# Kernel tuning notes

Hardware: AMD Instinct MI355X
Metric: run time of the kernel (lower is better)

The kernel has to match this reference:

```python
import jax, jax.numpy as jnp
import numpy as np

B, N, C, L, O = 32, 16000, 128, 512, 35
FS = 16000
F_LO, F_HI = 100.0, 8000.0
BETA = 0.9        # Leaky decay (snntorch Leaky beta)
AN_UTH = 0.5      # auditory-nerve threshold (an_uth)
TH = 1.0          # default threshold for later stages
STELI_STD = (1.0, 2.0, 3.0)


def _gammatone_kernels():
    # 4th-order gammatone impulse responses, ERB-spaced center freqs.
    erb = lambda f: 21.4 * np.log10(4.37 * f / 1000.0 + 1.0)
    erb_inv = lambda e: (10 ** (e / 21.4) - 1.0) * 1000.0 / 4.37
    cfs = erb_inv(np.linspace(erb(F_LO), erb(F_HI), C))          # [C]
    t = np.arange(L) / FS                                        # [L]
    bw = 1.019 * 24.7 * (4.37 * cfs / 1000.0 + 1.0)              # [C]
    g = (t[None, :] ** 3) * np.exp(-2 * np.pi * bw[:, None] * t[None, :]) \
        * np.cos(2 * np.pi * cfs[:, None] * t[None, :])          # [C,L]
    g = g / np.maximum(np.linalg.norm(g, axis=1, keepdims=True), 1e-12)
    return jnp.asarray(g, dtype=jnp.float32)


def _gauss_w(std, n):
    # fixed Gaussian lateral connectivity (OSF / stellate layer)
    i = np.arange(n, dtype=np.float64)
    w = np.exp(-((i[:, None] - i[None, :]) ** 2) / (2.0 * std ** 2))
    w = w / w.sum(axis=1, keepdims=True)
    return jnp.asarray(w, dtype=jnp.float32)


@jax.custom_vjp
def spike(x):
    return (x > 0).astype(x.dtype)

def _spk_fwd(x):
    return spike(x), x

def _spk_bwd(x, g):
    # ATan-style surrogate gradient (snntorch default)
    return (g / (1.0 + (jnp.pi * x) ** 2),)

spike.defvjp(_spk_fwd, _spk_bwd)


def setup_inputs() -> dict:
    key = jax.random.key(0)
    ks = jax.random.split(key, 8)
    s = 1.0 / np.sqrt(C)
    return {
        "audio": jax.random.normal(ks[0], (B, N), jnp.float32),
        "gt_kernels": _gammatone_kernels(),
        "W_an": jax.random.normal(ks[1], (C, C), jnp.float32) * s,
        "b_an": jnp.zeros((C,), jnp.float32),
        "W_b": _gauss_w(STELI_STD[0], C),
        "W_m": _gauss_w(STELI_STD[1], C),
        "W_n": _gauss_w(STELI_STD[2], C),
        "W_ic": jax.random.normal(ks[2], (C, C), jnp.float32) * s,
        "b_ic": jnp.zeros((C,), jnp.float32),
        "W_ac": jax.random.normal(ks[3], (O, C), jnp.float32) * s,
        "b_ac": jnp.zeros((O,), jnp.float32),
        "ihc_win": 160,
    }


def reference(audio, gt_kernels, W_an, b_an, W_b, W_m, W_n, W_ic, b_ic, W_ac, b_ac, ihc_win):
    # Cochlea: gammatone FIR filterbank.  [B,N] -> [B,C,N]
    x = jax.lax.conv_general_dilated(
        audio[:, None, :], gt_kernels[:, None, :], (1,), "SAME",
        dimension_numbers=("NCH", "OIH", "NCH"))
    # Inner hair cell: half-wave rectify + windowed average (envelope, downsample)
    x = jax.nn.relu(x)
    T = N // ihc_win
    x = x[..., : T * ihc_win].reshape(B, C, T, ihc_win).mean(-1)   # [B,C,T]
    x = x.transpose(2, 0, 1)                                       # [T,B,C]

    def leaky(mem, cur, th):
        mem = BETA * mem + cur
        spk = spike(mem - th)
        return spk, mem - spk * th   # reset by subtraction

    def step(carry, xt):
        m_an, m_b, m_m, m_n, m_ic, m_ac = carry
        s_an, m_an = leaky(m_an, xt @ W_an.T + b_an, AN_UTH)
        s_b,  m_b  = leaky(m_b,  s_an @ W_b.T, TH)
        s_m,  m_m  = leaky(m_m,  s_b @ W_m.T, TH)
        s_n,  m_n  = leaky(m_n,  s_m @ W_n.T, TH)
        s_ic, m_ic = leaky(m_ic, s_n @ W_ic.T + b_ic, TH)
        s_ac, m_ac = leaky(m_ac, s_ic @ W_ac.T + b_ac, TH)
        return (m_an, m_b, m_m, m_n, m_ic, m_ac), (s_ac, m_ac)

    z = jnp.zeros((B, C), x.dtype)
    za = jnp.zeros((B, O), x.dtype)
    _, (spk_rec, mem_rec) = jax.lax.scan(step, (z, z, z, z, z, za), x)
    # [T,B,O] -> [B,T,O]; stack (spk, mem) like the torch module's tuple output
    return jnp.stack([spk_rec.transpose(1, 0, 2), mem_rec.transpose(1, 0, 2)])
```

## Files before the change

### kernel.cpp

```cpp
#include <hip/hip_runtime.h>
#include <math.h>

#define BB 32
#define NN 16000
#define CC 128
#define LL 512
#define OO 35
#define TT 100
#define BTO (BB * TT * OO)
#define FSR 16000.0

#define SEG 640
#define NSEG 25
#define SPAN 1153

#define WT_OFF   0
#define PAR_OFF  0x100000
#define CUR_OFF  0
#define XT_OFF   0x350000

__global__ __launch_bounds__(512) void gt_tables(double* __restrict__ Wt,
                                                 double* __restrict__ par) {
    const int c = blockIdx.x;
    const int l = threadIdx.x;
    const double TWO_PI = 6.283185307179586476925287;
    const double e_lo = 21.4 * log10(4.37 * 100.0 / 1000.0 + 1.0);
    const double e_hi = 21.4 * log10(4.37 * 8000.0 / 1000.0 + 1.0);
    const double step = (e_hi - e_lo) / 127.0;
    const double e = (c == 127) ? e_hi : e_lo + c * step;
    const double cf = (pow(10.0, e / 21.4) - 1.0) * 1000.0 / 4.37;
    const double bw = 1.019 * 24.7 * (4.37 * cf / 1000.0 + 1.0);

    const double t = (double)l / FSR;
    const double env = exp(-TWO_PI * bw * t);
    const double ang = TWO_PI * cf * t;
    const double wr = env * cos(ang);
    const double wi = env * sin(ang);
    Wt[(l * CC + c) * 2 + 0] = wr;
    Wt[(l * CC + c) * 2 + 1] = wi;

    __shared__ double red[512];
    const double l3 = (double)l * (double)l * (double)l;
    const double q = l3 * wr;
    red[l] = q * q;
    __syncthreads();
    for (int s = 256; s > 0; s >>= 1) {
        if (l < s) red[l] += red[l + s];
        __syncthreads();
    }
    if (l == 0) {
        double* p = par + c * 16;
        const double a1 = TWO_PI * bw / FSR, th1 = TWO_PI * cf / FSR;
        const double e1 = exp(-a1);
        p[0] = e1 * cos(th1);
        p[1] = e1 * sin(th1);
        const double aL = TWO_PI * bw * (512.0 / FSR), thL = TWO_PI * cf * (512.0 / FSR);
        const double eL = exp(-aL);
        const double pr = eL * cos(thL), pim = eL * sin(thL);
        p[2] = pr;              p[3] = pim;
        p[4] = 512.0 * pr;      p[5] = 512.0 * pim;
        p[6] = 130816.0 * pr;   p[7] = 130816.0 * pim;
        p[8] = 22238720.0 * pr; p[9] = 22238720.0 * pim;
        p[10] = 1.0 / sqrt(red[0]);
    }
}

__global__ __launch_bounds__(128) void conv_rec(
    const float* __restrict__ audio,
    const double* __restrict__ Wt,
    const double* __restrict__ par,
    float* __restrict__ xt)
{
    const int blk = blockIdx.x;
    const int b = blk / NSEG;
    const int seg = blk % NSEG;
    const int n0 = seg * SEG;
    const int c = threadIdx.x;

    __shared__ float alds[SPAN];
    for (int i = c; i < SPAN; i += 128) {
        const int g = n0 - 256 + i;
        alds[i] = (g >= 0 && g < NN) ? audio[b * NN + g] : 0.0f;
    }
    __syncthreads();

    const double* p = par + c * 16;
    const double rr = p[0], ri = p[1];
    const double cr0 = p[2], ci0 = p[3], cr1 = p[4], ci1 = p[5];
    const double cr2 = p[6], ci2 = p[7], cr3 = p[8], ci3 = p[9];
    const double scale = p[10];

    double d0r = 0, d0i = 0, d1r = 0, d1i = 0, d2r = 0, d2i = 0, d3r = 0, d3i = 0;
    #pragma unroll 4
    for (int l = 0; l < 512; ++l) {
        const double wr = Wt[(l * CC + c) * 2 + 0];
        const double wi = Wt[(l * CC + c) * 2 + 1];
        const double av = (double)alds[SEG + 1 + l];
        const double bl = (double)l;
        const double b2 = bl * (bl - 1.0) * 0.5;
        const double b3 = b2 * (bl - 2.0) * (1.0 / 3.0);
        d0r = fma(wr, av, d0r);              d0i = fma(wi, av, d0i);
        const double t1 = av * bl;
        d1r = fma(wr, t1, d1r);              d1i = fma(wi, t1, d1i);
        const double t2 = av * b2;
        d2r = fma(wr, t2, d2r);              d2i = fma(wi, t2, d2i);
        const double t3 = av * b3;
        d3r = fma(wr, t3, d3r);              d3i = fma(wi, t3, d3i);
    }

    double wsum = 0.0;
    int widx = (b * TT + seg * 4 + 3) * CC + c;
    int cnt = 0;
    #pragma unroll 2
    for (int m = 0; m < SEG; ++m) {
        const int li = SEG - m;
        const double ain  = (double)alds[li];
        const double aout = (double)alds[li + 512];
        const double t3r = d3r + d2r, t3i = d3i + d2i;
        const double t2r = d2r + d1r, t2i = d2i + d1i;
        const double t1r = d1r + d0r, t1i = d1i + d0i;
        d3r = fma(t3r, rr, fma(t3i, -ri, -cr3 * aout));
        d3i = fma(t3r, ri, fma(t3i,  rr, -ci3 * aout));
        d2r = fma(t2r, rr, fma(t2i, -ri, -cr2 * aout));
        d2i = fma(t2r, ri, fma(t2i,  rr, -ci2 * aout));
        d1r = fma(t1r, rr, fma(t1i, -ri, -cr1 * aout));
        d1i = fma(t1r, ri, fma(t1i,  rr, -ci1 * aout));
        const double o0r = fma(d0r, rr, fma(d0i, -ri, fma(-cr0, aout, ain)));
        const double o0i = fma(d0r, ri, fma(d0i,  rr, -ci0 * aout));
        d0r = o0r; d0i = o0i;
        const double yv = scale * fma(6.0, d2r + d3r, d1r);
        float yf = (float)yv;
        yf = yf > 0.0f ? yf : 0.0f;
        wsum += (double)yf;
        if (++cnt == 160) {
            xt[widx] = (float)(wsum / 160.0);
            widx -= CC;
            wsum = 0.0;
            cnt = 0;
        }
    }
}

__global__ __launch_bounds__(128) void an_cur_kernel(
    const float* __restrict__ xt, const float* __restrict__ W_an,
    const float* __restrict__ b_an, double* __restrict__ cur_d)
{
    __shared__ float xr[CC];
    const int row = blockIdx.x;
    const int c = threadIdx.x;
    xr[c] = xt[row * CC + c];
    __syncthreads();
    const float* wr = W_an + c * CC;
    double acc = (double)b_an[c];
    #pragma unroll
    for (int k = 0; k < CC; k += 4) {
        float4 w4 = *reinterpret_cast<const float4*>(wr + k);
        acc += (double)w4.x * (double)xr[k]
             + (double)w4.y * (double)xr[k+1]
             + (double)w4.z * (double)xr[k+2]
             + (double)w4.w * (double)xr[k+3];
    }
    cur_d[row * CC + c] = acc;
}

#define R1 8
#define W1 17
#define R2 16
#define W2 33
#define R3 24
#define W3 49
#define SPW 24

__global__ __launch_bounds__(512, 1) void snn_kernel(
    const double* __restrict__ cur_an,
    const float* __restrict__ W_b, const float* __restrict__ W_m, const float* __restrict__ W_n,
    const float* __restrict__ W_ic, const float* __restrict__ b_ic,
    const float* __restrict__ W_ac, const float* __restrict__ b_ac,
    float* __restrict__ out)
{
    __shared__ __align__(16) float sa[2][176], sb[2][176], sm[2][176];
    __shared__ __align__(16) float sn_[2][CC];
    __shared__ __align__(16) double icp[2][4][CC];
    __shared__ __align__(16) float sic[2][CC];
    __shared__ double acp[2][2][36];
    __shared__ __align__(16) float wac[OO][132];

    const int b = blockIdx.x;
    const int tid = threadIdx.x;
    const int wid = tid >> 6;
    const int l = tid & 63;
    const int c0 = 2 * l, c1 = 2 * l + 1;

    {
        float* z0 = &sa[0][0]; float* z1 = &sb[0][0]; float* z2 = &sm[0][0];
        for (int i = tid; i < 352; i += 512) { z0[i] = 0.f; z1[i] = 0.f; z2[i] = 0.f; }
    }
    for (int i = tid; i < OO * CC; i += 512)
        wac[i >> 7][i & 127] = W_ac[i];

    float wband[2 * W3];
    double bic0 = 0.0, bic1 = 0.0, bacv = 0.0;
    double mm0 = 0.0, mm1 = 0.0;
    double mic0 = 0.0, mic1 = 0.0;
    double macv = 0.0;
    double2 pf0 = make_double2(0.0, 0.0), pf1 = make_double2(0.0, 0.0);

    if (wid == 0) {
        pf0 = *reinterpret_cast<const double2*>(&cur_an[(b * TT + 0) * CC + c0]);
        pf1 = *reinterpret_cast<const double2*>(&cur_an[(b * TT + 1) * CC + c0]);
        bic0 = (double)b_ic[c0]; bic1 = (double)b_ic[c1];
        if (l < OO) bacv = (double)b_ac[l];
    } else if (wid == 1) {
        #pragma unroll
        for (int x = 0; x < W1; ++x) {
            int k0 = c0 - R1 + x, k1 = c1 - R1 + x;
            wband[x]      = (k0 >= 0 && k0 < CC) ? W_b[c0 * CC + k0] : 0.f;
            wband[W1 + x] = (k1 >= 0 && k1 < CC) ? W_b[c1 * CC + k1] : 0.f;
        }
    } else if (wid == 2) {
        #pragma unroll
        for (int x = 0; x < W2; ++x) {
            int k0 = c0 - R2 + x, k1 = c1 - R2 + x;
            wband[x]      = (k0 >= 0 && k0 < CC) ? W_m[c0 * CC + k0] : 0.f;
            wband[W2 + x] = (k1 >= 0 && k1 < CC) ? W_m[c1 * CC + k1] : 0.f;
        }
    } else if (wid == 3) {
        #pragma unroll
        for (int x = 0; x < W3; ++x) {
            int k0 = c0 - R3 + x, k1 = c1 - R3 + x;
            wband[x]      = (k0 >= 0 && k0 < CC) ? W_n[c0 * CC + k0] : 0.f;
            wband[W3 + x] = (k1 >= 0 && k1 < CC) ? W_n[c1 * CC + k1] : 0.f;
        }
    } else {
        const int q = wid - 4;
        #pragma unroll
        for (int j = 0; j < 32; ++j) {
            wband[j]      = W_ic[c0 * CC + 32 * q + j];
            wband[32 + j] = W_ic[c1 * CC + 32 * q + j];
        }
    }
    __syncthreads();

    for (int tick = 0; tick < TT + 7; ++tick) {
        if (wid == 0) {
            if (tick < TT) {
                double2 cv = pf0; pf0 = pf1;
                if (tick + 2 < TT)
                    pf1 = *reinterpret_cast<const double2*>(&cur_an[(b * TT + tick + 2) * CC + c0]);
                double me0 = 0.9 * mm0 + cv.x; double d0 = me0 - 0.5;
                bool s0 = d0 > 0.0; mm0 = s0 ? d0 : me0;
                double me1 = 0.9 * mm1 + cv.y; double d1 = me1 - 0.5;
                bool s1 = d1 > 0.0; mm1 = s1 ? d1 : me1;
                *reinterpret_cast<float2*>(&sa[tick & 1][SPW + c0]) =
                    make_float2(s0 ? 1.f : 0.f, s1 ? 1.f : 0.f);
            }
            const int t5 = tick - 5;
            if (t5 >= 0 && t5 < TT) {
                const int p = t5 & 1;
                double2 q0 = *reinterpret_cast<const double2*>(&icp[p][0][c0]);
                double2 q1 = *reinterpret_cast<const double2*>(&icp[p][1][c0]);
                double2 q2 = *reinterpret_cast<const double2*>(&icp[p][2][c0]);
                double2 q3 = *reinterpret_cast<const double2*>(&icp[p][3][c0]);
                double acc0 = ((q0.x + q1.x) + (q2.x + q3.x)) + bic0;
                double acc1 = ((q0.y + q1.y) + (q2.y + q3.y)) + bic1;
                double mem0 = 0.9 * mic0 + acc0; double dd0 = mem0 - 1.0;
                bool s0 = dd0 > 0.0; mic0 = s0 ? dd0 : mem0;
                double mem1 = 0.9 * mic1 + acc1; double dd1 = mem1 - 1.0;
                bool s1 = dd1 > 0.0; mic1 = s1 ? dd1 : mem1;
                *reinterpret_cast<float2*>(&sic[p][c0]) =
                    make_float2(s0 ? 1.f : 0.f, s1 ? 1.f : 0.f);
            }
            const int t7 = tick - 7;
            if (l < OO && t7 >= 0 && t7 < TT) {
                const int p = t7 & 1;
                double acc = (acp[p][0][l] + acp[p][1][l]) + bacv;
                double mem = 0.9 * macv + acc;
                double d = mem - 1.0; bool s = d > 0.0;
                macv = s ? d : mem;
                const int idx = (b * TT + t7) * OO + l;
                out[idx] = s ? 1.f : 0.f;
                out[BTO + idx] = (float)macv;
            }
        } else if (wid == 1) {
            const int t = tick - 1;
            if (t >= 0 && t < TT) {
                const int p = t & 1;
                const float2* pw = reinterpret_cast<const float2*>(&sa[p][SPW + c0 - R1]);
                double aA0 = 0, aA1 = 0, aB0 = 0, aB1 = 0;
                #pragma unroll
                for (int i = 0; i < 9; ++i) {
                    float2 v = pw[i];
                    double vx = (double)v.x, vy = (double)v.y;
                    if (2 * i < W1)     aA0 = fma((double)wband[2 * i],          vx, aA0);
                    if (2 * i + 1 < W1) aA1 = fma((double)wband[2 * i + 1],      vy, aA1);
                    if (2 * i >= 1)     aB0 = fma((double)wband[W1 + 2 * i - 1], vx, aB0);
                    if (2 * i < W1)     aB1 = fma((double)wband[W1 + 2 * i],     vy, aB1);
                }
                double me0 = 0.9 * mm0 + (aA0 + aA1); double d0 = me0 - 1.0;
                bool s0 = d0 > 0.0; mm0 = s0 ? d0 : me0;
                double me1 = 0.9 * mm1 + (aB0 + aB1); double d1 = me1 - 1.0;
                bool s1 = d1 > 0.0; mm1 = s1 ? d1 : me1;
                *reinterpret_cast<float2*>(&sb[p][SPW + c0]) =
                    make_float2(s0 ? 1.f : 0.f, s1 ? 1.f : 0.f);
            }
            const int t6 = tick - 6;
            if (t6 >= 0 && t6 < TT) {
                const int p = t6 & 1, r = l >> 1, h = l & 1;
                const float* sp = &sic[p][h * 64];
                const float* wr = &wac[r][h * 64];
                double a0 = 0, a1 = 0, a2 = 0, a3 = 0;
                #pragma unroll
                for (int k = 0; k < 64; k += 4) {
                    float4 v = *reinterpret_cast<const float4*>(&sp[k]);
                    float4 w = *reinterpret_cast<const float4*>(&wr[k]);
                    a0 = fma((double)w.x, (double)v.x, a0);
                    a1 = fma((double)w.y, (double)v.y, a1);
                    a2 = fma((double)w.z, (double)v.z, a2);
                    a3 = fma((double)w.w, (double)v.w, a3);
                }
                acp[p][h][r] = (a0 + a1) + (a2 + a3);
            }
        } else if (wid == 2) {
            const int t = tick - 2;
            if (t >= 0 && t < TT) {
                const int p = t & 1;
                const float2* pw = reinterpret_cast<const float2*>(&sb[p][SPW + c0 - R2]);
                double aA0 = 0, aA1 = 0, aB0 = 0, aB1 = 0;
                #pragma unroll
                for (int i = 0; i < 17; ++i) {
                    float2 v = pw[i];
                    double vx = (double)v.x, vy = (double)v.y;
                    if (2 * i < W2)     aA0 = fma((double)wband[2 * i],          vx, aA0);
                    if (2 * i + 1 < W2) aA1 = fma((double)wband[2 * i + 1],      vy, aA1);
                    if (2 * i >= 1)     aB0 = fma((double)wband[W2 + 2 * i - 1], vx, aB0);
                    if (2 * i < W2)     aB1 = fma((double)wband[W2 + 2 * i],     vy, aB1);
                }
                double me0 = 0.9 * mm0 + (aA0 + aA1); double d0 = me0 - 1.0;
                bool s0 = d0 > 0.0; mm0 = s0 ? d0 : me0;
                double me1 = 0.9 * mm1 + (aB0 + aB1); double d1 = me1 - 1.0;
                bool s1 = d1 > 0.0; mm1 = s1 ? d1 : me1;
                *reinterpret_cast<float2*>(&sm[p][SPW + c0]) =
                    make_float2(s0 ? 1.f : 0.f, s1 ? 1.f : 0.f);
            }
            const int t6 = tick - 6;
            if (l < 6 && t6 >= 0 && t6 < TT) {
                const int p = t6 & 1, r = 32 + (l >> 1), h = l & 1;
                const float* sp = &sic[p][h * 64];
                const float* wr = &wac[r][h * 64];
                double a0 = 0, a1 = 0, a2 = 0, a3 = 0;
                #pragma unroll
                for (int k = 0; k < 64; k += 4) {
                    float4 v = *reinterpret_cast<const float4*>(&sp[k]);
                    float4 w = *reinterpret_cast<const float4*>(&wr[k]);
                    a0 = fma((double)w.x, (double)v.x, a0);
                    a1 = fma((double)w.y, (double)v.y, a1);
                    a2 = fma((double)w.z, (double)v.z, a2);
                    a3 = fma((double)w.w, (double)v.w, a3);
                }
                acp[p][h][r] = (a0 + a1) + (a2 + a3);
            }
        } else if (wid == 3) {
            const int t = tick - 3;
            if (t >= 0 && t < TT) {
                const int p = t & 1;
                const float2* pw = reinterpret_cast<const float2*>(&sm[p][SPW + c0 - R3]);
                double aA0 = 0, aA1 = 0, aB0 = 0, aB1 = 0;
                #pragma unroll
                for (int i = 0; i < 25; ++i) {
                    float2 v = pw[i];
                    double vx = (double)v.x, vy = (double)v.y;
                    if (2 * i < W3)     aA0 = fma((double)wband[2 * i],          vx, aA0);
                    if (2 * i + 1 < W3) aA1 = fma((double)wband[2 * i + 1],      vy, aA1);
                    if (2 * i >= 1)     aB0 = fma((double)wband[W3 + 2 * i - 1], vx, aB0);
                    if (2 * i < W3)     aB1 = fma((double)wband[W3 + 2 * i],     vy, aB1);
                }
                double me0 = 0.9 * mm0 + (aA0 + aA1); double d0 = me0 - 1.0;
                bool s0 = d0 > 0.0; mm0 = s0 ? d0 : me0;
                double me1 = 0.9 * mm1 + (aB0 + aB1); double d1 = me1 - 1.0;
                bool s1 = d1 > 0.0; mm1 = s1 ? d1 : me1;
                *reinterpret_cast<float2*>(&sn_[p][c0]) =
                    make_float2(s0 ? 1.f : 0.f, s1 ? 1.f : 0.f);
            }
        } else {
            const int t = tick - 4;
            if (t >= 0 && t < TT) {
                const int p = t & 1, q = wid - 4;
                const float* sp = &sn_[p][32 * q];
                double a0 = 0, a1 = 0, g0 = 0, g1 = 0;
                #pragma unroll
                for (int k = 0; k < 32; k += 4) {
                    float4 v = *reinterpret_cast<const float4*>(&sp[k]);
                    a0 = fma((double)wband[k],          (double)v.x, a0);
                    a1 = fma((double)wband[k + 1],      (double)v.y, a1);
                    a0 = fma((double)wband[k + 2],      (double)v.z, a0);
                    a1 = fma((double)wband[k + 3],      (double)v.w, a1);
                    g0 = fma((double)wband[32 + k],     (double)v.x, g0);
                    g1 = fma((double)wband[32 + k + 1], (double)v.y, g1);
                    g0 = fma((double)wband[32 + k + 2], (double)v.z, g0);
                    g1 = fma((double)wband[32 + k + 3], (double)v.w, g1);
                }
                *reinterpret_cast<double2*>(&icp[p][q][c0]) =
                    make_double2(a0 + a1, g0 + g1);
            }
        }
        __syncthreads();
    }
}

extern "C" void kernel_launch(void* const* d_in, const int* in_sizes, int n_in,
                              void* d_out, int out_size, void* d_ws, size_t ws_size,
                              hipStream_t stream) {
    const float* audio = (const float*)d_in[0];
    const float* W_an  = (const float*)d_in[2];
    const float* b_an  = (const float*)d_in[3];
    const float* W_b   = (const float*)d_in[4];
    const float* W_m   = (const float*)d_in[5];
    const float* W_n   = (const float*)d_in[6];
    const float* W_ic  = (const float*)d_in[7];
    const float* b_ic  = (const float*)d_in[8];
    const float* W_ac  = (const float*)d_in[9];
    const float* b_ac  = (const float*)d_in[10];

    char* ws = (char*)d_ws;
    double* Wt    = (double*)(ws + WT_OFF);
    double* par   = (double*)(ws + PAR_OFF);
    double* cur_d = (double*)(ws + CUR_OFF);
    float*  xt    = (float*)(ws + XT_OFF);
    float*  out   = (float*)d_out;

    gt_tables<<<dim3(CC), dim3(512), 0, stream>>>(Wt, par);
    conv_rec<<<dim3(BB * NSEG), dim3(128), 0, stream>>>(audio, Wt, par, xt);
    an_cur_kernel<<<dim3(BB * TT), dim3(128), 0, stream>>>(xt, W_an, b_an, cur_d);
    snn_kernel<<<dim3(BB), dim3(512), 0, stream>>>(
        cur_d, W_b, W_m, W_n, W_ic, b_ic, W_ac, b_ac, out);
}
```

Measured before the change: 330.9 us.

## Store SNN spikes and W_ac as double in LDS, strength-reduce binomial weights

In the gammatone init loop the binomial coefficients are now updated incrementally instead of being recomputed per tap, and the complex weight pair is read with one double2 load. The recursion loop unroll goes from 2 to 4. In the SNN kernel the shared spike buffers and W_ac copy are widened to double, which removes float-to-double conversions in the inner products. The leftover W_ac rows are moved from warp 2 to warp 0. The cost is double the LDS footprint and bandwidth for those buffers.

```diff
diff --git a/kernel.cpp b/kernel.cpp
--- a/kernel.cpp
+++ b/kernel.cpp
@@ -91,27 +91,25 @@
     const double scale = p[10];
 
     double d0r = 0, d0i = 0, d1r = 0, d1i = 0, d2r = 0, d2i = 0, d3r = 0, d3i = 0;
+    double b1 = 0.0, b2 = 0.0, b3 = 0.0;
     #pragma unroll 4
     for (int l = 0; l < 512; ++l) {
-        const double wr = Wt[(l * CC + c) * 2 + 0];
-        const double wi = Wt[(l * CC + c) * 2 + 1];
+        const double2 w = *reinterpret_cast<const double2*>(&Wt[(l * CC + c) * 2]);
         const double av = (double)alds[SEG + 1 + l];
-        const double bl = (double)l;
-        const double b2 = bl * (bl - 1.0) * 0.5;
-        const double b3 = b2 * (bl - 2.0) * (1.0 / 3.0);
-        d0r = fma(wr, av, d0r);              d0i = fma(wi, av, d0i);
-        const double t1 = av * bl;
-        d1r = fma(wr, t1, d1r);              d1i = fma(wi, t1, d1i);
+        d0r = fma(w.x, av, d0r);             d0i = fma(w.y, av, d0i);
+        const double t1 = av * b1;
+        d1r = fma(w.x, t1, d1r);             d1i = fma(w.y, t1, d1i);
         const double t2 = av * b2;
-        d2r = fma(wr, t2, d2r);              d2i = fma(wi, t2, d2i);
+        d2r = fma(w.x, t2, d2r);             d2i = fma(w.y, t2, d2i);
         const double t3 = av * b3;
-        d3r = fma(wr, t3, d3r);              d3i = fma(wi, t3, d3i);
+        d3r = fma(w.x, t3, d3r);             d3i = fma(w.y, t3, d3i);
+        b3 += b2; b2 += b1; b1 += 1.0;
     }
 
     double wsum = 0.0;
     int widx = (b * TT + seg * 4 + 3) * CC + c;
     int cnt = 0;
-    #pragma unroll 2
+    #pragma unroll 4
     for (int m = 0; m < SEG; ++m) {
         const int li = SEG - m;
         const double ain  = (double)alds[li];
@@ -178,12 +176,12 @@
     const float* __restrict__ W_ac, const float* __restrict__ b_ac,
     float* __restrict__ out)
 {
-    __shared__ __align__(16) float sa[2][176], sb[2][176], sm[2][176];
-    __shared__ __align__(16) float sn_[2][CC];
+    __shared__ __align__(16) double sa[2][176], sb[2][176], sm[2][176];
+    __shared__ __align__(16) double sn_[2][CC];
     __shared__ __align__(16) double icp[2][4][CC];
-    __shared__ __align__(16) float sic[2][CC];
+    __shared__ __align__(16) double sic[2][CC];
     __shared__ double acp[2][2][36];
-    __shared__ __align__(16) float wac[OO][132];
+    __shared__ __align__(16) double wacd[OO][132];
 
     const int b = blockIdx.x;
     const int tid = threadIdx.x;
@@ -192,11 +190,11 @@
     const int c0 = 2 * l, c1 = 2 * l + 1;
 
     {
-        float* z0 = &sa[0][0]; float* z1 = &sb[0][0]; float* z2 = &sm[0][0];
-        for (int i = tid; i < 352; i += 512) { z0[i] = 0.f; z1[i] = 0.f; z2[i] = 0.f; }
+        double* z0 = &sa[0][0]; double* z1 = &sb[0][0]; double* z2 = &sm[0][0];
+        for (int i = tid; i < 352; i += 512) { z0[i] = 0.0; z1[i] = 0.0; z2[i] = 0.0; }
     }
     for (int i = tid; i < OO * CC; i += 512)
-        wac[i >> 7][i & 127] = W_ac[i];
+        wacd[i >> 7][i & 127] = (double)W_ac[i];
 
     float wband[2 * W3];
     double bic0 = 0.0, bic1 = 0.0, bacv = 0.0;
@@ -251,8 +249,8 @@
                 bool s0 = d0 > 0.0; mm0 = s0 ? d0 : me0;
                 double me1 = 0.9 * mm1 + cv.y; double d1 = me1 - 0.5;
                 bool s1 = d1 > 0.0; mm1 = s1 ? d1 : me1;
-                *reinterpret_cast<float2*>(&sa[tick & 1][SPW + c0]) =
-                    make_float2(s0 ? 1.f : 0.f, s1 ? 1.f : 0.f);
+                *reinterpret_cast<double2*>(&sa[tick & 1][SPW + c0]) =
+                    make_double2(s0 ? 1.0 : 0.0, s1 ? 1.0 : 0.0);
             }
             const int t5 = tick - 5;
             if (t5 >= 0 && t5 < TT) {
@@ -267,8 +265,27 @@
                 bool s0 = dd0 > 0.0; mic0 = s0 ? dd0 : mem0;
                 double mem1 = 0.9 * mic1 + acc1; double dd1 = mem1 - 1.0;
                 bool s1 = dd1 > 0.0; mic1 = s1 ? dd1 : mem1;
-                *reinterpret_cast<float2*>(&sic[p][c0]) =
-                    make_float2(s0 ? 1.f : 0.f, s1 ? 1.f : 0.f);
+                *reinterpret_cast<double2*>(&sic[p][c0]) =
+                    make_double2(s0 ? 1.0 : 0.0, s1 ? 1.0 : 0.0);
+            }
+            const int t6 = tick - 6;
+            if (l < 6 && t6 >= 0 && t6 < TT) {
+                const int p = t6 & 1, r = 32 + (l >> 1), h = l & 1;
+                const double* sp = &sic[p][h * 64];
+                const double* wr = &wacd[r][h * 64];
+                double a0 = 0, a1 = 0, a2 = 0, a3 = 0;
+                #pragma unroll
+                for (int k = 0; k < 64; k += 4) {
+                    double2 v01 = *reinterpret_cast<const double2*>(&sp[k]);
+                    double2 v23 = *reinterpret_cast<const double2*>(&sp[k + 2]);
+                    double2 w01 = *reinterpret_cast<const double2*>(&wr[k]);
+                    double2 w23 = *reinterpret_cast<const double2*>(&wr[k + 2]);
+                    a0 = fma(w01.x, v01.x, a0);
+                    a1 = fma(w01.y, v01.y, a1);
+                    a2 = fma(w23.x, v23.x, a2);
+                    a3 = fma(w23.y, v23.y, a3);
+                }
+                acp[p][h][r] = (a0 + a1) + (a2 + a3);
             }
             const int t7 = tick - 7;
             if (l < OO && t7 >= 0 && t7 < TT) {
@@ -285,12 +302,12 @@
             const int t = tick - 1;
             if (t >= 0 && t < TT) {
                 const int p = t & 1;
-                const float2* pw = reinterpret_cast<const float2*>(&sa[p][SPW + c0 - R1]);
+                const double2* pw = reinterpret_cast<const double2*>(&sa[p][SPW + c0 - R1]);
                 double aA0 = 0, aA1 = 0, aB0 = 0, aB1 = 0;
                 #pragma unroll
                 for (int i = 0; i < 9; ++i) {
-                    float2 v = pw[i];
-                    double vx = (double)v.x, vy = (double)v.y;
+                    double2 v = pw[i];
+                    double vx = v.x, vy = v.y;
                     if (2 * i < W1)     aA0 = fma((double)wband[2 * i],          vx, aA0);
                     if (2 * i + 1 < W1) aA1 = fma((double)wband[2 * i + 1],      vy, aA1);
                     if (2 * i >= 1)     aB0 = fma((double)wband[W1 + 2 * i - 1], vx, aB0);
@@ -300,23 +317,25 @@
                 bool s0 = d0 > 0.0; mm0 = s0 ? d0 : me0;
                 double me1 = 0.9 * mm1 + (aB0 + aB1); double d1 = me1 - 1.0;
                 bool s1 = d1 > 0.0; mm1 = s1 ? d1 : me1;
-                *reinterpret_cast<float2*>(&sb[p][SPW + c0]) =
-                    make_float2(s0 ? 1.f : 0.f, s1 ? 1.f : 0.f);
+                *reinterpret_cast<double2*>(&sb[p][SPW + c0]) =
+                    make_double2(s0 ? 1.0 : 0.0, s1 ? 1.0 : 0.0);
             }
             const int t6 = tick - 6;
             if (t6 >= 0 && t6 < TT) {
                 const int p = t6 & 1, r = l >> 1, h = l & 1;
-                const float* sp = &sic[p][h * 64];
-                const float* wr = &wac[r][h * 64];
+                const double* sp = &sic[p][h * 64];
+                const double* wr = &wacd[r][h * 64];
                 double a0 = 0, a1 = 0, a2 = 0, a3 = 0;
                 #pragma unroll
                 for (int k = 0; k < 64; k += 4) {
-                    float4 v = *reinterpret_cast<const float4*>(&sp[k]);
-                    float4 w = *reinterpret_cast<const float4*>(&wr[k]);
-                    a0 = fma((double)w.x, (double)v.x, a0);
-                    a1 = fma((double)w.y, (double)v.y, a1);
-                    a2 = fma((double)w.z, (double)v.z, a2);
-                    a3 = fma((double)w.w, (double)v.w, a3);
+                    double2 v01 = *reinterpret_cast<const double2*>(&sp[k]);
+                    double2 v23 = *reinterpret_cast<const double2*>(&sp[k + 2]);
+                    double2 w01 = *reinterpret_cast<const double2*>(&wr[k]);
+                    double2 w23 = *reinterpret_cast<const double2*>(&wr[k + 2]);
+                    a0 = fma(w01.x, v01.x, a0);
+                    a1 = fma(w01.y, v01.y, a1);
+                    a2 = fma(w23.x, v23.x, a2);
+                    a3 = fma(w23.y, v23.y, a3);
                 }
                 acp[p][h][r] = (a0 + a1) + (a2 + a3);
             }
@@ -324,12 +343,12 @@
             const int t = tick - 2;
             if (t >= 0 && t < TT) {
                 const int p = t & 1;
-                const float2* pw = reinterpret_cast<const float2*>(&sb[p][SPW + c0 - R2]);
+                const double2* pw = reinterpret_cast<const double2*>(&sb[p][SPW + c0 - R2]);
                 double aA0 = 0, aA1 = 0, aB0 = 0, aB1 = 0;
                 #pragma unroll
                 for (int i = 0; i < 17; ++i) {
-                    float2 v = pw[i];
-                    double vx = (double)v.x, vy = (double)v.y;
+                    double2 v = pw[i];
+                    double vx = v.x, vy = v.y;
                     if (2 * i < W2)     aA0 = fma((double)wband[2 * i],          vx, aA0);
                     if (2 * i + 1 < W2) aA1 = fma((double)wband[2 * i + 1],      vy, aA1);
                     if (2 * i >= 1)     aB0 = fma((double)wband[W2 + 2 * i - 1], vx, aB0);
@@ -339,36 +358,19 @@
                 bool s0 = d0 > 0.0; mm0 = s0 ? d0 : me0;
                 double me1 = 0.9 * mm1 + (aB0 + aB1); double d1 = me1 - 1.0;
                 bool s1 = d1 > 0.0; mm1 = s1 ? d1 : me1;
-                *reinterpret_cast<float2*>(&sm[p][SPW + c0]) =
-                    make_float2(s0 ? 1.f : 0.f, s1 ? 1.f : 0.f);
-            }
-            const int t6 = tick - 6;
-            if (l < 6 && t6 >= 0 && t6 < TT) {
-                const int p = t6 & 1, r = 32 + (l >> 1), h = l & 1;
-                const float* sp = &sic[p][h * 64];
-                const float* wr = &wac[r][h * 64];
-                double a0 = 0, a1 = 0, a2 = 0, a3 = 0;
-                #pragma unroll
-                for (int k = 0; k < 64; k += 4) {
-                    float4 v = *reinterpret_cast<const float4*>(&sp[k]);
-                    float4 w = *reinterpret_cast<const float4*>(&wr[k]);
-                    a0 = fma((double)w.x, (double)v.x, a0);
-                    a1 = fma((double)w.y, (double)v.y, a1);
-                    a2 = fma((double)w.z, (double)v.z, a2);
-                    a3 = fma((double)w.w, (double)v.w, a3);
-                }
-                acp[p][h][r] = (a0 + a1) + (a2 + a3);
+                *reinterpret_cast<double2*>(&sm[p][SPW + c0]) =
+                    make_double2(s0 ? 1.0 : 0.0, s1 ? 1.0 : 0.0);
             }
         } else if (wid == 3) {
             const int t = tick - 3;
             if (t >= 0 && t < TT) {
                 const int p = t & 1;
-                const float2* pw = reinterpret_cast<const float2*>(&sm[p][SPW + c0 - R3]);
+                const double2* pw = reinterpret_cast<const double2*>(&sm[p][SPW + c0 - R3]);
                 double aA0 = 0, aA1 = 0, aB0 = 0, aB1 = 0;
                 #pragma unroll
                 for (int i = 0; i < 25; ++i) {
-                    float2 v = pw[i];
-                    double vx = (double)v.x, vy = (double)v.y;
+                    double2 v = pw[i];
+                    double vx = v.x, vy = v.y;
                     if (2 * i < W3)     aA0 = fma((double)wband[2 * i],          vx, aA0);
                     if (2 * i + 1 < W3) aA1 = fma((double)wband[2 * i + 1],      vy, aA1);
                     if (2 * i >= 1)     aB0 = fma((double)wband[W3 + 2 * i - 1], vx, aB0);
@@ -378,26 +380,27 @@
                 bool s0 = d0 > 0.0; mm0 = s0 ? d0 : me0;
                 double me1 = 0.9 * mm1 + (aB0 + aB1); double d1 = me1 - 1.0;
                 bool s1 = d1 > 0.0; mm1 = s1 ? d1 : me1;
-                *reinterpret_cast<float2*>(&sn_[p][c0]) =
-                    make_float2(s0 ? 1.f : 0.f, s1 ? 1.f : 0.f);
+                *reinterpret_cast<double2*>(&sn_[p][c0]) =
+                    make_double2(s0 ? 1.0 : 0.0, s1 ? 1.0 : 0.0);
             }
         } else {
             const int t = tick - 4;
             if (t >= 0 && t < TT) {
                 const int p = t & 1, q = wid - 4;
-                const float* sp = &sn_[p][32 * q];
+                const double* sp = &sn_[p][32 * q];
                 double a0 = 0, a1 = 0, g0 = 0, g1 = 0;
                 #pragma unroll
                 for (int k = 0; k < 32; k += 4) {
-                    float4 v = *reinterpret_cast<const float4*>(&sp[k]);
-                    a0 = fma((double)wband[k],          (double)v.x, a0);
-                    a1 = fma((double)wband[k + 1],      (double)v.y, a1);
-                    a0 = fma((double)wband[k + 2],      (double)v.z, a0);
-                    a1 = fma((double)wband[k + 3],      (double)v.w, a1);
-                    g0 = fma((double)wband[32 + k],     (double)v.x, g0);
-                    g1 = fma((double)wband[32 + k + 1], (double)v.y, g1);
-                    g0 = fma((double)wband[32 + k + 2], (double)v.z, g0);
-                    g1 = fma((double)wband[32 + k + 3], (double)v.w, g1);
+                    double2 va = *reinterpret_cast<const double2*>(&sp[k]);
+                    double2 vb = *reinterpret_cast<const double2*>(&sp[k + 2]);
+                    a0 = fma((double)wband[k],          va.x, a0);
+                    a1 = fma((double)wband[k + 1],      va.y, a1);
+                    a0 = fma((double)wband[k + 2],      vb.x, a0);
+                    a1 = fma((double)wband[k + 3],      vb.y, a1);
+                    g0 = fma((double)wband[32 + k],     va.x, g0);
+                    g1 = fma((double)wband[32 + k + 1], va.y, g1);
+                    g0 = fma((double)wband[32 + k + 2], vb.x, g0);
+                    g1 = fma((double)wband[32 + k + 3], vb.y, g1);
                 }
                 *reinterpret_cast<double2*>(&icp[p][q][c0]) =
                     make_double2(a0 + a1, g0 + g1);
```

Measured after the change: 309.9 us. 6.3% less time.
